# Performance work log

Measured on AMD Instinct MI355X. Metric: run time of the kernel, lower is better.

## Reference

```python
import jax, jax.numpy as jnp
import numpy as np

B, N, D = 16, 512, 256
HEADS = 8
HIDEF = 1024
BLOCK, WINDOW = 32, 64
LEVELS = 5
PYOUT = 128
NCLS, NANCH = 5, 9
NEG = -1e9


def _sinusoidal_pos(n, d):
    # PositionEmbeddingStatic: deterministic sinusoidal table [n, d]
    pos = np.arange(n)[:, None].astype(np.float64)
    i = np.arange(d)[None, :]
    angle = pos / np.power(10000.0, (2 * (i // 2)) / d)
    pe = np.where(i % 2 == 0, np.sin(angle), np.cos(angle))
    return jnp.asarray(pe, jnp.float32)


def _layernorm(x, g, b, eps=1e-5):
    m = x.mean(-1, keepdims=True)
    v = x.var(-1, keepdims=True)
    return (x - m) * jax.lax.rsqrt(v + eps) * g + b


def _bn(x_bcn, g, b, eps=1e-5):
    # BatchNorm1d in training mode: per-channel batch stats over (B, N)
    m = x_bcn.mean((0, 2), keepdims=True)
    v = x_bcn.var((0, 2), keepdims=True)
    return (x_bcn - m) * jax.lax.rsqrt(v + eps) * g[None, :, None] + b[None, :, None]


def _sparse_attention(x, Wqkv, bqkv, Wo, bo):
    # Windowed block-sparse attention: queries in block i attend to key blocks
    # [i-w, i+w] with w = window_size // block_size. Never materializes SxS.
    Bx, Nx, Dx = x.shape
    H, dh = HEADS, Dx // HEADS
    nb, bs = Nx // BLOCK, BLOCK
    w = WINDOW // BLOCK
    qkv = x @ Wqkv + bqkv
    q, k, v = jnp.split(qkv, 3, axis=-1)

    def to_blocks(t):  # [B,N,D] -> [B,H,nb,bs,dh]
        return t.reshape(Bx, nb, bs, H, dh).transpose(0, 3, 1, 2, 4)

    q, k, v = to_blocks(q), to_blocks(k), to_blocks(v)
    offs = list(range(-w, w + 1))
    # roll by -o puts key block (i+o) at query-block position i
    k_band = jnp.concatenate([jnp.roll(k, -o, axis=2) for o in offs], axis=3)
    v_band = jnp.concatenate([jnp.roll(v, -o, axis=2) for o in offs], axis=3)
    blk = jnp.arange(nb)
    valid = jnp.concatenate(
        [jnp.repeat(((blk + o >= 0) & (blk + o < nb))[:, None], bs, axis=1) for o in offs],
        axis=1)  # [nb, (2w+1)*bs]
    scale = 1.0 / jnp.sqrt(jnp.asarray(dh, x.dtype))
    scores = jnp.einsum('bhnqd,bhnkd->bhnqk', q, k_band) * scale
    scores = jnp.where(valid[None, None, :, None, :], scores, NEG)
    p = jax.nn.softmax(scores, axis=-1)
    o = jnp.einsum('bhnqk,bhnkd->bhnqd', p, v_band)
    o = o.transpose(0, 2, 3, 1, 4).reshape(Bx, Nx, Dx)
    return o @ Wo + bo


def setup_inputs():
    key = jax.random.key(0)
    ks = iter(jax.random.split(key, 48))
    g = lambda shape, s=0.02: jax.random.normal(next(ks), shape, jnp.float32) * s
    z = lambda *shape: jnp.zeros(shape, jnp.float32)
    o = lambda *shape: jnp.ones(shape, jnp.float32)
    return {
        'x': jax.random.normal(next(ks), (B, N, D), jnp.float32),
        'patch_W': g((D, D)), 'patch_b': z(D),
        'ln_g': o(D), 'ln_b': z(D),
        'ff_W1': g((D, HIDEF)), 'ff_b1': z(HIDEF),
        'ff_W2': g((HIDEF, D)), 'ff_b2': z(D),
        'Wqkv': g((D, 3 * D)), 'bqkv': z(3 * D),
        'Wo': g((D, D)), 'bo': z(D),
        'bn1_g': o(D), 'bn1_b': z(D),
        'bn2_g': o(D), 'bn2_b': z(D),
        'pyr_W': g((LEVELS, D, PYOUT)), 'pyr_b': z(LEVELS, PYOUT),
        'fcl_W': g((LEVELS * PYOUT * N, 128), 0.005), 'fcl_b': z(128),
        'addbn_g': o(128), 'addbn_b': z(128),
        'cls_W1': g((128, 256)), 'cls_b1': z(256),
        'cls_W2': g((256, NCLS * NANCH)), 'cls_b2': z(NCLS * NANCH),
        'box_W1': g((128, 128)), 'box_b1': z(128),
        'box_W2': g((128, 4 * NANCH)), 'box_b2': z(4 * NANCH),
    }


def reference(x, patch_W, patch_b, ln_g, ln_b, ff_W1, ff_b1, ff_W2, ff_b2,
              Wqkv, bqkv, Wo, bo, bn1_g, bn1_b, bn2_g, bn2_b,
              pyr_W, pyr_b, fcl_W, fcl_b, addbn_g, addbn_b,
              cls_W1, cls_b1, cls_W2, cls_b2, box_W1, box_b1, box_W2, box_b2):
    pos = _sinusoidal_pos(N, D)

    def ff(h):
        return jax.nn.gelu(h @ ff_W1 + ff_b1) @ ff_W2 + ff_b2

    def mnt(h):
        h = _layernorm(h @ patch_W + patch_b, ln_g, ln_b)  # patch embed + norm
        h = h + pos[None]
        idt = h
        h = ff(h)
        h = _sparse_attention(h, Wqkv, bqkv, Wo, bo)
        h = h + idt
        h = _bn(h.transpose(0, 2, 1), bn1_g, bn1_b).transpose(0, 2, 1)
        idt = h
        h = ff(h) + idt
        h = _bn(h.transpose(0, 2, 1), bn2_g, bn2_b).transpose(0, 2, 1)
        return h

    outs = []
    for _ in range(5):
        x = mnt(x)
        outs.append(x.transpose(0, 2, 1))  # [B, D, N]

    # pyramid: per-level 1x1 conv D -> 128
    feats = [jnp.einsum('bdn,dc->bcn', outs[i], pyr_W[i]) + pyr_b[i][None, :, None]
             for i in range(LEVELS)]
    flat = jnp.concatenate([f.reshape(f.shape[0], -1) for f in feats], axis=1)
    add = (flat @ fcl_W + fcl_b)[:, :, None]          # [B,128,1]
    add = _bn(add, addbn_g, addbn_b).transpose(0, 2, 1)  # [B,1,128]
    cls = jax.nn.relu(add @ cls_W1 + cls_b1) @ cls_W2 + cls_b2
    cls = jax.nn.softmax(cls, axis=-1).reshape(-1, NANCH, NCLS)  # eval mode softmax
    box = (jax.nn.relu(add @ box_W1 + box_b1) @ box_W2 + box_b2).reshape(-1, NANCH, 4)
    return jnp.concatenate([cls, box], axis=-1)  # [B, NANCH, NCLS+4]
```

## Files before the change

kernel.cpp:

```cpp
#include <hip/hip_runtime.h>
#include <hip/hip_bf16.h>
#include <math.h>

#define B_ 16
#define N_ 512
#define D_ 256
#define HEADS_ 8
#define DH_ 32
#define HIDEF_ 1024
#define NBLK_ 16
#define BS_ 32
#define LEVELS_ 5
#define PYOUT_ 128
#define ROWS_ (B_ * N_)
#define FCL_K 327680
#define FCL_KB 256
#define FCL_CHUNKS 1280

typedef __attribute__((ext_vector_type(8))) short short8;
typedef __attribute__((ext_vector_type(4))) short short4v;
typedef __attribute__((ext_vector_type(4))) unsigned short ushort4v;
typedef __attribute__((ext_vector_type(4))) float f32x4;

__device__ __forceinline__ float bf2f(short u) {
    return __uint_as_float(((unsigned int)(unsigned short)u) << 16);
}
__device__ __forceinline__ unsigned short f2bf(float x) {
    __hip_bfloat16 h = __float2bfloat16(x);
    return *reinterpret_cast<unsigned short*>(&h);
}

__global__ void pos_kernel(float* __restrict__ pos) {
    int idx = blockIdx.x * 256 + threadIdx.x;
    if (idx >= N_ * D_) return;
    int n = idx >> 8, i = idx & 255;
    double angle = (double)n / pow(10000.0, (double)(2 * (i >> 1)) / 256.0);
    pos[idx] = (float)((i & 1) ? cos(angle) : sin(angle));
}

__device__ __forceinline__ float gelu_f(float x) {
    float x3 = x * x * x;
    return 0.5f * x * (1.f + tanhf(0.7978845608028654f * (x + 0.044715f * x3)));
}

__global__ void tobf16_kernel(const float* __restrict__ x, __hip_bfloat16* __restrict__ y, int n) {
    int i = blockIdx.x * 256 + threadIdx.x;
    if (i < n) y[i] = __float2bfloat16(x[i]);
}

__global__ __launch_bounds__(256) void wconv_kernel(const float* __restrict__ W,
                                                    __hip_bfloat16* __restrict__ Wt,
                                                    int K, int N) {
    int z = blockIdx.z;
    const float* Wz = W + (size_t)z * K * N;
    __hip_bfloat16* Wtz = Wt + (size_t)z * K * N;
    __shared__ float t[32][33];
    int bx = blockIdx.x * 32, by = blockIdx.y * 32;
    int tx = threadIdx.x, ty = threadIdx.y;
#pragma unroll
    for (int i = 0; i < 32; i += 8)
        t[ty + i][tx] = Wz[(size_t)(by + ty + i) * N + bx + tx];
    __syncthreads();
#pragma unroll
    for (int i = 0; i < 32; i += 8)
        Wtz[(size_t)(bx + ty + i) * K + by + tx] = __float2bfloat16(t[tx][ty + i]);
}

template <int ACT, bool OUTF, bool OUTB, bool SCAT, bool STATS, int BN>
__global__ __launch_bounds__(256) void bgemm_kernel(
    const __hip_bfloat16* __restrict__ A, const __hip_bfloat16* __restrict__ Wt,
    const float* __restrict__ bias, const float* __restrict__ resid,
    float* __restrict__ C, __hip_bfloat16* __restrict__ Cb, int M, int Nn, int K,
    int level, float* __restrict__ bnp) {
    __shared__ __hip_bfloat16 Alds[128 * 32];
    __shared__ __hip_bfloat16 Blds[BN * 32];
    constexpr int MW = (BN == 128) ? 4 : 2;
    constexpr int WH = (BN == 128) ? 64 : 32;
    constexpr int BR = BN / 64;
    int tid = threadIdx.x;
    int wid = tid >> 6, lane = tid & 63;
    int row0 = blockIdx.y * 128, col0 = blockIdx.x * BN;
    int wr = (BN == 128) ? (wid >> 1) : wid;
    int wc = (BN == 128) ? (wid & 1) : 0;
    int r16 = lane & 15, kq = lane >> 4;
    int rdoff = kq ^ ((r16 >> 1) & 3);

    f32x4 acc[MW][4];
#pragma unroll
    for (int m = 0; m < MW; m++)
#pragma unroll
        for (int n = 0; n < 4; n++) acc[m][n] = (f32x4){0.f, 0.f, 0.f, 0.f};

    for (int k0 = 0; k0 < K; k0 += 32) {
#pragma unroll
        for (int i = 0; i < 2; i++) {
            int slot = i * 256 + tid;
            int row = slot >> 2, qp = slot & 3;
            int q = qp ^ ((row >> 1) & 3);
            const __hip_bfloat16* ga = A + (size_t)(row0 + row) * K + k0 + q * 8;
            __builtin_amdgcn_global_load_lds(
                (const __attribute__((address_space(1))) void*)ga,
                (__attribute__((address_space(3))) void*)((char*)Alds + i * 4096 + wid * 1024),
                16, 0, 0);
        }
#pragma unroll
        for (int i = 0; i < BR; i++) {
            int slot = i * 256 + tid;
            int row = slot >> 2, qp = slot & 3;
            int q = qp ^ ((row >> 1) & 3);
            const __hip_bfloat16* gb = Wt + (size_t)(col0 + row) * K + k0 + q * 8;
            __builtin_amdgcn_global_load_lds(
                (const __attribute__((address_space(1))) void*)gb,
                (__attribute__((address_space(3))) void*)((char*)Blds + i * 4096 + wid * 1024),
                16, 0, 0);
        }
        __syncthreads();
        short8 af[MW], bf[4];
#pragma unroll
        for (int m = 0; m < MW; m++) {
            int row = wr * WH + m * 16 + r16;
            af[m] = *reinterpret_cast<const short8*>(
                reinterpret_cast<const char*>(Alds) + row * 64 + rdoff * 16);
        }
#pragma unroll
        for (int n = 0; n < 4; n++) {
            int row = wc * 64 + n * 16 + r16;
            bf[n] = *reinterpret_cast<const short8*>(
                reinterpret_cast<const char*>(Blds) + row * 64 + rdoff * 16);
        }
#pragma unroll
        for (int m = 0; m < MW; m++)
#pragma unroll
            for (int n = 0; n < 4; n++)
                acc[m][n] = __builtin_amdgcn_mfma_f32_16x16x32_bf16(af[m], bf[n], acc[m][n], 0, 0, 0);
        __syncthreads();
    }

    int rg = lane >> 4;
    float s1a[4] = {0.f, 0.f, 0.f, 0.f}, s2a[4] = {0.f, 0.f, 0.f, 0.f};
    if (SCAT) {
#pragma unroll
        for (int n = 0; n < 4; n++) {
            int cc = col0 + wc * 64 + n * 16 + r16;
            int bb = cc >> 9, nn = cc & 511;
            float* dst = C + (size_t)bb * (LEVELS_ * PYOUT_ * N_) +
                         (size_t)level * PYOUT_ * N_ + nn;
#pragma unroll
            for (int m = 0; m < MW; m++) {
                int rbase = wr * WH + m * 16 + rg * 4;
#pragma unroll
                for (int j = 0; j < 4; j++) {
                    int ch = rbase + j;
                    dst[(size_t)ch * N_] = acc[m][n][j] + bias[ch];
                }
            }
        }
    } else {
#pragma unroll
        for (int n = 0; n < 4; n++) {
            int cc = col0 + wc * 64 + n * 16 + r16;
            float bv = bias[cc];
#pragma unroll
            for (int m = 0; m < MW; m++) {
                int rb = row0 + wr * WH + m * 16 + rg * 4;
#pragma unroll
                for (int j = 0; j < 4; j++) {
                    int r = rb + j;
                    float v = acc[m][n][j] + bv;
                    if (resid) v += resid[(size_t)r * Nn + cc];
                    if (ACT == 1) v = gelu_f(v);
                    if (OUTF) C[(size_t)r * Nn + cc] = v;
                    if (OUTB) Cb[(size_t)r * Nn + cc] = __float2bfloat16(v);
                    if (STATS) { s1a[n] += v; s2a[n] += v * v; }
                }
            }
        }
    }
    if (STATS) {
        float* sc = (float*)Alds;
        int part = wid * 4 + rg;
#pragma unroll
        for (int n = 0; n < 4; n++) {
            int c = wc * 64 + n * 16 + r16;
            sc[c * 16 + part] = s1a[n];
            sc[1024 + c * 16 + part] = s2a[n];
        }
        __syncthreads();
        if (tid < BN) {
            float a = 0.f, b2 = 0.f;
#pragma unroll
            for (int p = 0; p < 16; p++) {
                a += sc[tid * 16 + p];
                b2 += sc[1024 + tid * 16 + p];
            }
            bnp[blockIdx.y * 256 + col0 + tid] = a;
            bnp[16384 + blockIdx.y * 256 + col0 + tid] = b2;
        }
    }
}

__global__ __launch_bounds__(256) void patchln_kernel(
    const __hip_bfloat16* __restrict__ A, const __hip_bfloat16* __restrict__ Wt,
    const float* __restrict__ bias, const float* __restrict__ lng,
    const float* __restrict__ lnb, const float* __restrict__ pos,
    float* __restrict__ H, __hip_bfloat16* __restrict__ Hb) {
    __shared__ char __attribute__((aligned(16))) smem[33280];
    __hip_bfloat16* Alds = (__hip_bfloat16*)smem;
    __hip_bfloat16* Blds = (__hip_bfloat16*)(smem + 2048);
    float (*Cls)[260] = (float(*)[260])smem;
    int tid = threadIdx.x;
    int wid = tid >> 6, lane = tid & 63;
    int row0 = blockIdx.x * 32;
    int r16 = lane & 15, kq = lane >> 4, g = lane >> 4;
    int rdoff = kq ^ ((r16 >> 1) & 3);

    f32x4 acc[2][4];
#pragma unroll
    for (int m = 0; m < 2; m++)
#pragma unroll
        for (int n = 0; n < 4; n++) acc[m][n] = (f32x4){0.f, 0.f, 0.f, 0.f};

    for (int k0 = 0; k0 < 256; k0 += 32) {
        if (tid < 128) {
            int row = tid >> 2, qp = tid & 3;
            int q = qp ^ ((row >> 1) & 3);
            const __hip_bfloat16* ga = A + (size_t)(row0 + row) * 256 + k0 + q * 8;
            __builtin_amdgcn_global_load_lds(
                (const __attribute__((address_space(1))) void*)ga,
                (__attribute__((address_space(3))) void*)((char*)Alds + wid * 1024),
                16, 0, 0);
        }
#pragma unroll
        for (int i = 0; i < 4; i++) {
            int slot = i * 256 + tid;
            int row = slot >> 2, qp = slot & 3;
            int q = qp ^ ((row >> 1) & 3);
            const __hip_bfloat16* gb = Wt + (size_t)row * 256 + k0 + q * 8;
            __builtin_amdgcn_global_load_lds(
                (const __attribute__((address_space(1))) void*)gb,
                (__attribute__((address_space(3))) void*)((char*)Blds + i * 4096 + wid * 1024),
                16, 0, 0);
        }
        __syncthreads();
        short8 af[2], bf[4];
#pragma unroll
        for (int m = 0; m < 2; m++) {
            int row = m * 16 + r16;
            af[m] = *reinterpret_cast<const short8*>(
                reinterpret_cast<const char*>(Alds) + row * 64 + rdoff * 16);
        }
#pragma unroll
        for (int n = 0; n < 4; n++) {
            int row = wid * 64 + n * 16 + r16;
            bf[n] = *reinterpret_cast<const short8*>(
                reinterpret_cast<const char*>(Blds) + row * 64 + rdoff * 16);
        }
#pragma unroll
        for (int m = 0; m < 2; m++)
#pragma unroll
            for (int n = 0; n < 4; n++)
                acc[m][n] = __builtin_amdgcn_mfma_f32_16x16x32_bf16(af[m], bf[n], acc[m][n], 0, 0, 0);
        __syncthreads();
    }
#pragma unroll
    for (int n = 0; n < 4; n++) {
        int col = wid * 64 + n * 16 + r16;
        float bv = bias[col];
#pragma unroll
        for (int m = 0; m < 2; m++)
#pragma unroll
            for (int j = 0; j < 4; j++)
                Cls[m * 16 + g * 4 + j][col] = acc[m][n][j] + bv;
    }
    __syncthreads();
    float4 g4 = ((const float4*)lng)[lane];
    float4 b4 = ((const float4*)lnb)[lane];
#pragma unroll
    for (int rr = 0; rr < 8; rr++) {
        int r = wid * 8 + rr;
        float4 v = *(const float4*)&Cls[r][lane * 4];
        float s = v.x + v.y + v.z + v.w;
#pragma unroll
        for (int mk = 32; mk; mk >>= 1) s += __shfl_xor(s, mk);
        float mean = s * (1.f / 256.f);
        float dx = v.x - mean, dy = v.y - mean, dz = v.z - mean, dw = v.w - mean;
        float q = dx * dx + dy * dy + dz * dz + dw * dw;
#pragma unroll
        for (int mk = 32; mk; mk >>= 1) q += __shfl_xor(q, mk);
        float rstd = rsqrtf(q * (1.f / 256.f) + 1e-5f);
        int grow = row0 + r;
        float4 p4 = ((const float4*)pos)[(size_t)(grow & (N_ - 1)) * 64 + lane];
        float o0 = dx * rstd * g4.x + b4.x + p4.x;
        float o1 = dy * rstd * g4.y + b4.y + p4.y;
        float o2 = dz * rstd * g4.z + b4.z + p4.z;
        float o3 = dw * rstd * g4.w + b4.w + p4.w;
        ((float4*)(H + (size_t)grow * D_))[lane] = (float4){o0, o1, o2, o3};
        ushort4v u = {f2bf(o0), f2bf(o1), f2bf(o2), f2bf(o3)};
        *((ushort4v*)(Hb + (size_t)grow * D_) + lane) = u;
    }
}

__global__ __launch_bounds__(256) void bn_applyfin_kernel(
    const float* __restrict__ x, const float* __restrict__ bnp,
    const float* __restrict__ g, const float* __restrict__ b,
    float* __restrict__ y, __hip_bfloat16* __restrict__ yb) {
    int tid = threadIdx.x;
    __shared__ float sm[256], sv[256];
    {
        float s = 0.f, s2 = 0.f;
#pragma unroll 4
        for (int yy = 0; yy < 64; yy++) {
            s += bnp[yy * 256 + tid];
            s2 += bnp[16384 + yy * 256 + tid];
        }
        float m = s * (1.f / 8192.f);
        sm[tid] = m;
        sv[tid] = rsqrtf(s2 * (1.f / 8192.f) - m * m + 1e-5f);
    }
    __syncthreads();
    int lane = tid & 63, w = tid >> 6;
    int row0 = blockIdx.x * 32;
    float4 m4 = *(const float4*)&sm[lane * 4];
    float4 r4 = *(const float4*)&sv[lane * 4];
    float4 g4 = ((const float4*)g)[lane];
    float4 b4 = ((const float4*)b)[lane];
#pragma unroll
    for (int rr = 0; rr < 8; rr++) {
        int row = row0 + w * 8 + rr;
        float4 x4 = ((const float4*)(x + (size_t)row * D_))[lane];
        float o0 = (x4.x - m4.x) * r4.x * g4.x + b4.x;
        float o1 = (x4.y - m4.y) * r4.y * g4.y + b4.y;
        float o2 = (x4.z - m4.z) * r4.z * g4.z + b4.z;
        float o3 = (x4.w - m4.w) * r4.w * g4.w + b4.w;
        if (y) ((float4*)(y + (size_t)row * D_))[lane] = (float4){o0, o1, o2, o3};
        if (yb) {
            ushort4v u = {f2bf(o0), f2bf(o1), f2bf(o2), f2bf(o3)};
            *((ushort4v*)(yb + (size_t)row * D_) + lane) = u;
        }
    }
}

__global__ __launch_bounds__(256) void attn_kernel(
    const __hip_bfloat16* __restrict__ qkv, __hip_bfloat16* __restrict__ outb) {
    int bx = blockIdx.x, h = blockIdx.y, b = blockIdx.z;
    int tid = threadIdx.x;
    int wid = tid >> 6, lane = tid & 63;
    __shared__ __hip_bfloat16 Klds[256 * 32];
    __shared__ __hip_bfloat16 Vt[32 * 264];
    const short* q16 = (const short*)qkv;

#pragma unroll
    for (int r = 0; r < 4; r++) {
        int slot = r * 256 + tid;
        int row = slot >> 2, qp = slot & 3;
        int ql = qp ^ ((row >> 1) & 3);
        int jb = bx * 4 - 2 + (row >> 5);
        jb = jb < 0 ? 0 : (jb > 15 ? 15 : jb);
        const short* ga = q16 + ((size_t)(b * N_ + jb * 32 + (row & 31))) * 768 + 256 + h * 32 + ql * 8;
        __builtin_amdgcn_global_load_lds(
            (const __attribute__((address_space(1))) void*)ga,
            (__attribute__((address_space(3))) void*)((char*)Klds + r * 4096 + wid * 1024),
            16, 0, 0);
    }
    {
        int row = tid;
        int jb = bx * 4 - 2 + (row >> 5);
        jb = jb < 0 ? 0 : (jb > 15 ? 15 : jb);
        const short* gv = q16 + ((size_t)(b * N_ + jb * 32 + (row & 31))) * 768 + 512 + h * 32;
        short8 v0 = *(const short8*)(gv);
        short8 v1 = *(const short8*)(gv + 8);
        short8 v2 = *(const short8*)(gv + 16);
        short8 v3 = *(const short8*)(gv + 24);
        short* vt = (short*)Vt;
#pragma unroll
        for (int e = 0; e < 8; e++) {
            vt[(e) * 264 + row] = v0[e];
            vt[(8 + e) * 264 + row] = v1[e];
            vt[(16 + e) * 264 + row] = v2[e];
            vt[(24 + e) * 264 + row] = v3[e];
        }
    }
    __syncthreads();

    int i = bx * 4 + wid;
    int c = lane & 15, g = lane >> 4;
    const float scale = 0.17677669529663687f;

#pragma unroll
    for (int qt = 0; qt < 2; qt++) {
        const short* qa = q16 + ((size_t)(b * N_ + i * 32 + qt * 16 + c)) * 768 + h * 32 + g * 8;
        short8 bq = *(const short8*)qa;
        f32x4 st[10];
#pragma unroll
        for (int t = 0; t < 10; t++) {
            int jb = i - 2 + (t >> 1);
            if (jb >= 0 && jb < NBLK_) {
                int row = wid * 32 + t * 16 + c;
                int phys = g ^ ((row >> 1) & 3);
                short8 ak = *(const short8*)((const char*)Klds + row * 64 + phys * 16);
                st[t] = __builtin_amdgcn_mfma_f32_16x16x32_bf16(
                    ak, bq, (f32x4){0.f, 0.f, 0.f, 0.f}, 0, 0, 0);
            }
        }
        float mx = -1e30f;
#pragma unroll
        for (int t = 0; t < 10; t++) {
            int jb = i - 2 + (t >> 1);
            if (jb >= 0 && jb < NBLK_) {
#pragma unroll
                for (int j = 0; j < 4; j++) {
                    st[t][j] *= scale;
                    mx = fmaxf(mx, st[t][j]);
                }
            }
        }
        mx = fmaxf(mx, __shfl_xor(mx, 16));
        mx = fmaxf(mx, __shfl_xor(mx, 32));
        float sum = 0.f;
#pragma unroll
        for (int t = 0; t < 10; t++) {
            int jb = i - 2 + (t >> 1);
            if (jb >= 0 && jb < NBLK_) {
#pragma unroll
                for (int j = 0; j < 4; j++) {
                    float e = __expf(st[t][j] - mx);
                    st[t][j] = e;
                    sum += e;
                }
            }
        }
        sum += __shfl_xor(sum, 16);
        sum += __shfl_xor(sum, 32);
        float inv = 1.f / sum;
        f32x4 o0 = (f32x4){0.f, 0.f, 0.f, 0.f};
        f32x4 o1 = (f32x4){0.f, 0.f, 0.f, 0.f};
        const short* vt = (const short*)Vt;
#pragma unroll
        for (int t = 0; t < 10; t++) {
            int jb = i - 2 + (t >> 1);
            if (jb >= 0 && jb < NBLK_) {
                short8 pa = (short8)0;
#pragma unroll
                for (int j = 0; j < 4; j++) pa[j] = (short)f2bf(st[t][j] * inv);
                int kb = wid * 32 + t * 16 + g * 4;
                short4v vb0 = *(const short4v*)(vt + (0 * 16 + c) * 264 + kb);
                short4v vb1 = *(const short4v*)(vt + (1 * 16 + c) * 264 + kb);
                short8 b0 = (short8)0, b1 = (short8)0;
#pragma unroll
                for (int e = 0; e < 4; e++) { b0[e] = vb0[e]; b1[e] = vb1[e]; }
                o0 = __builtin_amdgcn_mfma_f32_16x16x32_bf16(pa, b0, o0, 0, 0, 0);
                o1 = __builtin_amdgcn_mfma_f32_16x16x32_bf16(pa, b1, o1, 0, 0, 0);
            }
        }
#pragma unroll
        for (int j = 0; j < 4; j++) {
            size_t rbase = ((size_t)(b * N_ + i * 32 + qt * 16 + g * 4 + j)) * D_ + h * DH_;
            outb[rbase + c] = __float2bfloat16(o0[j]);
            outb[rbase + 16 + c] = __float2bfloat16(o1[j]);
        }
    }
}

__global__ __launch_bounds__(256) void fcl_partial_kernel(
    const float* __restrict__ flat, const float* __restrict__ W,
    float* __restrict__ partial) {
    int chunk = blockIdx.x;
    int t = threadIdx.x;
    int k0 = chunk * FCL_KB;
    __shared__ float fl[FCL_KB][20];
#pragma unroll
    for (int b = 0; b < 16; b++)
        fl[t][b] = flat[(size_t)b * FCL_K + k0 + t];
    __syncthreads();
    int j = t & 127, bg = t >> 7;
    f32x4 a0 = (f32x4){0.f, 0.f, 0.f, 0.f};
    f32x4 a1 = (f32x4){0.f, 0.f, 0.f, 0.f};
#pragma unroll 8
    for (int k = 0; k < FCL_KB; k++) {
        float w = W[(size_t)(k0 + k) * 128 + j];
        f32x4 f0 = *(const f32x4*)&fl[k][bg * 8];
        f32x4 f1 = *(const f32x4*)&fl[k][bg * 8 + 4];
        a0 += f0 * w;
        a1 += f1 * w;
    }
#pragma unroll
    for (int bi = 0; bi < 4; bi++) {
        partial[((size_t)chunk * 16 + bg * 8 + bi) * 128 + j] = a0[bi];
        partial[((size_t)chunk * 16 + bg * 8 + 4 + bi) * 128 + j] = a1[bi];
    }
}

__global__ __launch_bounds__(256) void fcl_reduce_kernel(
    const float* __restrict__ partial, const float* __restrict__ fcl_b,
    float* __restrict__ add) {
    int c0 = blockIdx.x * 32;
    int t = threadIdx.x;
    int ry = t >> 5, cx = t & 31;
    float s = 0.f;
    for (int r = ry; r < FCL_CHUNKS; r += 8)
        s += partial[(size_t)r * 2048 + c0 + cx];
    __shared__ float red[8][32];
    red[ry][cx] = s; __syncthreads();
    if (ry == 0) {
        float tot = 0.f;
#pragma unroll
        for (int q = 0; q < 8; q++) tot += red[q][cx];
        int col = c0 + cx;
        add[col] = tot + fcl_b[col & 127];
    }
}

__global__ __launch_bounds__(256) void head_kernel(
    const float* __restrict__ add, const float* __restrict__ abg, const float* __restrict__ abb,
    const float* __restrict__ cls_W1, const float* __restrict__ cls_b1,
    const float* __restrict__ cls_W2, const float* __restrict__ cls_b2,
    const float* __restrict__ box_W1, const float* __restrict__ box_b1,
    const float* __restrict__ box_W2, const float* __restrict__ box_b2,
    float* __restrict__ out) {
    __shared__ float a2[16][128];
    __shared__ float cm[16][256];
    __shared__ float cls[16][45];
    __shared__ float bmid[16][128];
    __shared__ float smden[16];
    int t = threadIdx.x;
    if (t < 128) {
        float m = 0.f;
#pragma unroll
        for (int b = 0; b < 16; b++) m += add[b * 128 + t];
        m *= (1.f / 16.f);
        float v = 0.f;
#pragma unroll
        for (int b = 0; b < 16; b++) { float d = add[b * 128 + t] - m; v += d * d; }
        v *= (1.f / 16.f);
        float sc = rsqrtf(v + 1e-5f) * abg[t];
#pragma unroll
        for (int b = 0; b < 16; b++) a2[b][t] = (add[b * 128 + t] - m) * sc + abb[t];
    }
    __syncthreads();
    for (int idx = t; idx < 4096; idx += 256) {
        int m = idx >> 8, c = idx & 255;
        float a = cls_b1[c];
        for (int k = 0; k < 128; k++) a += a2[m][k] * cls_W1[k * 256 + c];
        cm[m][c] = fmaxf(a, 0.f);
    }
    for (int idx = t; idx < 2048; idx += 256) {
        int m = idx >> 7, c = idx & 127;
        float a = box_b1[c];
        for (int k = 0; k < 128; k++) a += a2[m][k] * box_W1[k * 128 + c];
        bmid[m][c] = fmaxf(a, 0.f);
    }
    __syncthreads();
    for (int idx = t; idx < 720; idx += 256) {
        int m = idx / 45, c = idx % 45;
        float a = cls_b2[c];
        for (int k = 0; k < 256; k++) a += cm[m][k] * cls_W2[k * 45 + c];
        cls[m][c] = a;
    }
    __syncthreads();
    if (t < 16) {
        float mx = -1e30f;
        for (int c = 0; c < 45; c++) mx = fmaxf(mx, cls[t][c]);
        float s = 0.f;
        for (int c = 0; c < 45; c++) { float e = expf(cls[t][c] - mx); cls[t][c] = e; s += e; }
        smden[t] = s;
    }
    for (int idx = t; idx < 576; idx += 256) {
        int m = idx / 36, c = idx % 36;
        float a = box_b2[c];
        for (int k = 0; k < 128; k++) a += bmid[m][k] * box_W2[k * 36 + c];
        out[m * 81 + (c >> 2) * 9 + 5 + (c & 3)] = a;
    }
    __syncthreads();
    for (int idx = t; idx < 720; idx += 256) {
        int m = idx / 45, c = idx % 45;
        out[m * 81 + (c / 5) * 9 + (c % 5)] = cls[m][c] / smden[m];
    }
}

extern "C" void kernel_launch(void* const* d_in, const int* in_sizes, int n_in,
                              void* d_out, int out_size, void* d_ws, size_t ws_size,
                              hipStream_t stream) {
    const float* x_in    = (const float*)d_in[0];
    const float* patch_W = (const float*)d_in[1];
    const float* patch_b = (const float*)d_in[2];
    const float* ln_g    = (const float*)d_in[3];
    const float* ln_b    = (const float*)d_in[4];
    const float* ff_W1   = (const float*)d_in[5];
    const float* ff_b1   = (const float*)d_in[6];
    const float* ff_W2   = (const float*)d_in[7];
    const float* ff_b2   = (const float*)d_in[8];
    const float* Wqkv    = (const float*)d_in[9];
    const float* bqkv    = (const float*)d_in[10];
    const float* Wo      = (const float*)d_in[11];
    const float* bo      = (const float*)d_in[12];
    const float* bn1_g   = (const float*)d_in[13];
    const float* bn1_b   = (const float*)d_in[14];
    const float* bn2_g   = (const float*)d_in[15];
    const float* bn2_b   = (const float*)d_in[16];
    const float* pyr_W   = (const float*)d_in[17];
    const float* pyr_b   = (const float*)d_in[18];
    const float* fcl_W   = (const float*)d_in[19];
    const float* fcl_b   = (const float*)d_in[20];
    const float* addbn_g = (const float*)d_in[21];
    const float* addbn_b = (const float*)d_in[22];
    const float* cls_W1  = (const float*)d_in[23];
    const float* cls_b1  = (const float*)d_in[24];
    const float* cls_W2  = (const float*)d_in[25];
    const float* cls_b2  = (const float*)d_in[26];
    const float* box_W1  = (const float*)d_in[27];
    const float* box_b1  = (const float*)d_in[28];
    const float* box_W2  = (const float*)d_in[29];
    const float* box_b2  = (const float*)d_in[30];
    float* out = (float*)d_out;

    float* ws = (float*)d_ws;
    size_t off = 0;
    float* POS   = ws + off; off += 131072;
    float* H     = ws + off; off += 2097152;
    float* T     = ws + off; off += 2097152;
    float* UNION = ws + off; off += 4194304;
    float* FLAT  = ws + off; off += 5242880;
    float* PART  = ws + off; off += (size_t)FCL_CHUNKS * 2048;
    float* STATS = ws + off; off += 512;
    float* BNP   = ws + off; off += 2 * 64 * 256;
    float* ADD   = ws + off; off += 2048;
    __hip_bfloat16* Hb   = (__hip_bfloat16*)(ws + off); off += 1048576;
    __hip_bfloat16* Tb   = (__hip_bfloat16*)(ws + off); off += 1048576;
    __hip_bfloat16* Xb   = (__hip_bfloat16*)(ws + off); off += 1048576;
    __hip_bfloat16* ATb  = (__hip_bfloat16*)(ws + off); off += 1048576;
    __hip_bfloat16* patchWt = (__hip_bfloat16*)(ws + off); off += 32768;
    __hip_bfloat16* qkvWt   = (__hip_bfloat16*)(ws + off); off += 98304;
    __hip_bfloat16* WoWt    = (__hip_bfloat16*)(ws + off); off += 32768;
    __hip_bfloat16* W1t     = (__hip_bfloat16*)(ws + off); off += 131072;
    __hip_bfloat16* W2t     = (__hip_bfloat16*)(ws + off); off += 131072;
    __hip_bfloat16* pyrWt   = (__hip_bfloat16*)(ws + off); off += 81920;
    __hip_bfloat16* MIDb = (__hip_bfloat16*)UNION;
    __hip_bfloat16* QKVb = (__hip_bfloat16*)UNION;
    (void)STATS;

    pos_kernel<<<(N_ * D_ + 255) / 256, 256, 0, stream>>>(POS);
    wconv_kernel<<<dim3(D_ / 32, D_ / 32, 1), dim3(32, 8), 0, stream>>>(patch_W, patchWt, D_, D_);
    wconv_kernel<<<dim3(768 / 32, D_ / 32, 1), dim3(32, 8), 0, stream>>>(Wqkv, qkvWt, D_, 768);
    wconv_kernel<<<dim3(D_ / 32, D_ / 32, 1), dim3(32, 8), 0, stream>>>(Wo, WoWt, D_, D_);
    wconv_kernel<<<dim3(HIDEF_ / 32, D_ / 32, 1), dim3(32, 8), 0, stream>>>(ff_W1, W1t, D_, HIDEF_);
    wconv_kernel<<<dim3(D_ / 32, HIDEF_ / 32, 1), dim3(32, 8), 0, stream>>>(ff_W2, W2t, HIDEF_, D_);
    wconv_kernel<<<dim3(PYOUT_ / 32, D_ / 32, LEVELS_), dim3(32, 8), 0, stream>>>(pyr_W, pyrWt, D_, PYOUT_);
    tobf16_kernel<<<(ROWS_ * D_ + 255) / 256, 256, 0, stream>>>(x_in, Xb, ROWS_ * D_);

    for (int it = 0; it < 5; it++) {
        patchln_kernel<<<256, 256, 0, stream>>>(Xb, patchWt, patch_b, ln_g, ln_b, POS, H, Hb);
        bgemm_kernel<1, false, true, false, false, 128><<<dim3(8, 64), 256, 0, stream>>>(
            Hb, W1t, ff_b1, nullptr, nullptr, MIDb, ROWS_, HIDEF_, D_, 0, nullptr);
        bgemm_kernel<0, false, true, false, false, 64><<<dim3(4, 64), 256, 0, stream>>>(
            MIDb, W2t, ff_b2, nullptr, nullptr, Tb, ROWS_, D_, HIDEF_, 0, nullptr);
        bgemm_kernel<0, false, true, false, false, 128><<<dim3(6, 64), 256, 0, stream>>>(
            Tb, qkvWt, bqkv, nullptr, nullptr, QKVb, ROWS_, 768, D_, 0, nullptr);
        attn_kernel<<<dim3(4, HEADS_, B_), 256, 0, stream>>>(QKVb, ATb);
        bgemm_kernel<0, true, false, false, true, 64><<<dim3(4, 64), 256, 0, stream>>>(
            ATb, WoWt, bo, H, T, nullptr, ROWS_, D_, D_, 0, BNP);
        bn_applyfin_kernel<<<256, 256, 0, stream>>>(T, BNP, bn1_g, bn1_b, H, Hb);
        bgemm_kernel<1, false, true, false, false, 128><<<dim3(8, 64), 256, 0, stream>>>(
            Hb, W1t, ff_b1, nullptr, nullptr, MIDb, ROWS_, HIDEF_, D_, 0, nullptr);
        bgemm_kernel<0, true, false, false, true, 64><<<dim3(4, 64), 256, 0, stream>>>(
            MIDb, W2t, ff_b2, H, T, nullptr, ROWS_, D_, HIDEF_, 0, BNP);
        bn_applyfin_kernel<<<256, 256, 0, stream>>>(T, BNP, bn2_g, bn2_b, nullptr, Xb);
        bgemm_kernel<0, false, false, true, false, 64><<<dim3(128, 1), 256, 0, stream>>>(
            pyrWt + (size_t)it * D_ * PYOUT_, Xb, pyr_b + it * PYOUT_, nullptr,
            FLAT, nullptr, PYOUT_, ROWS_, D_, it, nullptr);
    }

    fcl_partial_kernel<<<FCL_CHUNKS, 256, 0, stream>>>(FLAT, fcl_W, PART);
    fcl_reduce_kernel<<<64, 256, 0, stream>>>(PART, fcl_b, ADD);
    head_kernel<<<1, 256, 0, stream>>>(ADD, addbn_g, addbn_b,
        cls_W1, cls_b1, cls_W2, cls_b2, box_W1, box_b1, box_W2, box_b2, out);
    (void)in_sizes; (void)n_in; (void)out_size; (void)ws_size;
}
```

Baseline: 1.004 ms.

## Double GEMM K-tile to 64 and merge prep kernels into one launch

The bf16 GEMM and patch-LN kernels now stage 64-wide K tiles in LDS, with an 8-way XOR swizzle and two MFMA sub-steps per tile. This halves the number of barrier pairs and loop iterations per K pass, at the cost of more LDS per block, which can reduce occupancy. The eight setup launches (positional table, six weight transposes, input cast) are folded into a single prep kernel that dispatches by block index. The input cast is also vectorized.

```diff
diff --git a/kernel.cpp b/kernel.cpp
--- a/kernel.cpp
+++ b/kernel.cpp
@@ -30,40 +30,58 @@
     return *reinterpret_cast<unsigned short*>(&h);
 }
 
-__global__ void pos_kernel(float* __restrict__ pos) {
-    int idx = blockIdx.x * 256 + threadIdx.x;
-    if (idx >= N_ * D_) return;
-    int n = idx >> 8, i = idx & 255;
-    double angle = (double)n / pow(10000.0, (double)(2 * (i >> 1)) / 256.0);
-    pos[idx] = (float)((i & 1) ? cos(angle) : sin(angle));
-}
-
 __device__ __forceinline__ float gelu_f(float x) {
     float x3 = x * x * x;
     return 0.5f * x * (1.f + tanhf(0.7978845608028654f * (x + 0.044715f * x3)));
 }
 
-__global__ void tobf16_kernel(const float* __restrict__ x, __hip_bfloat16* __restrict__ y, int n) {
-    int i = blockIdx.x * 256 + threadIdx.x;
-    if (i < n) y[i] = __float2bfloat16(x[i]);
-}
-
-__global__ __launch_bounds__(256) void wconv_kernel(const float* __restrict__ W,
-                                                    __hip_bfloat16* __restrict__ Wt,
-                                                    int K, int N) {
-    int z = blockIdx.z;
-    const float* Wz = W + (size_t)z * K * N;
-    __hip_bfloat16* Wtz = Wt + (size_t)z * K * N;
-    __shared__ float t[32][33];
-    int bx = blockIdx.x * 32, by = blockIdx.y * 32;
-    int tx = threadIdx.x, ty = threadIdx.y;
+__global__ __launch_bounds__(256) void prep_kernel(
+    const float* __restrict__ patch_W, const float* __restrict__ Wqkv,
+    const float* __restrict__ Wo, const float* __restrict__ ff_W1,
+    const float* __restrict__ ff_W2, const float* __restrict__ pyr_W,
+    const float* __restrict__ x_in,
+    __hip_bfloat16* __restrict__ patchWt, __hip_bfloat16* __restrict__ qkvWt,
+    __hip_bfloat16* __restrict__ WoWt, __hip_bfloat16* __restrict__ W1t,
+    __hip_bfloat16* __restrict__ W2t, __hip_bfloat16* __restrict__ pyrWt,
+    float* __restrict__ pos, __hip_bfloat16* __restrict__ Xb) {
+    __shared__ float tt[32][33];
+    int bid = blockIdx.x, t = threadIdx.x;
+    if (bid >= 1504) {
+        int base = (bid - 1504) * 2048 + t * 8;
+        float4 a = *(const float4*)&x_in[base];
+        float4 b = *(const float4*)&x_in[base + 4];
+        ushort4v u0 = {f2bf(a.x), f2bf(a.y), f2bf(a.z), f2bf(a.w)};
+        ushort4v u1 = {f2bf(b.x), f2bf(b.y), f2bf(b.z), f2bf(b.w)};
+        *(ushort4v*)((short*)Xb + base) = u0;
+        *(ushort4v*)((short*)Xb + base + 4) = u1;
+        return;
+    }
+    if (bid >= 992) {
+        int idx = (bid - 992) * 256 + t;
+        int n = idx >> 8, i = idx & 255;
+        double angle = (double)n / pow(10000.0, (double)(2 * (i >> 1)) / 256.0);
+        pos[idx] = (float)((i & 1) ? cos(angle) : sin(angle));
+        return;
+    }
+    const float* W; __hip_bfloat16* Wt; int K, N, bx, by;
+    if (bid < 64)       { W = patch_W; Wt = patchWt; K = 256; N = 256; bx = bid % 8; by = bid / 8; }
+    else if (bid < 256) { int l = bid - 64;  W = Wqkv;  Wt = qkvWt; K = 256; N = 768;  bx = l % 24; by = l / 24; }
+    else if (bid < 320) { int l = bid - 256; W = Wo;    Wt = WoWt;  K = 256; N = 256;  bx = l % 8;  by = l / 8; }
+    else if (bid < 576) { int l = bid - 320; W = ff_W1; Wt = W1t;   K = 256; N = 1024; bx = l % 32; by = l / 32; }
+    else if (bid < 832) { int l = bid - 576; W = ff_W2; Wt = W2t;   K = 1024; N = 256; bx = l % 8;  by = l / 32 * 4 + (l / 8) % 4; }
+    else                { int l = bid - 832; int z = l / 32; int r = l % 32;
+                          W = pyr_W + (size_t)z * 256 * 128; Wt = pyrWt + (size_t)z * 256 * 128;
+                          K = 256; N = 128; bx = r % 4; by = r / 4; }
+    if (bid >= 576 && bid < 832) { int l = bid - 576; bx = l % 8; by = l / 8; }
+    int bx32 = bx * 32, by32 = by * 32;
+    int tx = t & 31, ty = t >> 5;
 #pragma unroll
     for (int i = 0; i < 32; i += 8)
-        t[ty + i][tx] = Wz[(size_t)(by + ty + i) * N + bx + tx];
+        tt[ty + i][tx] = W[(size_t)(by32 + ty + i) * N + bx32 + tx];
     __syncthreads();
 #pragma unroll
     for (int i = 0; i < 32; i += 8)
-        Wtz[(size_t)(bx + ty + i) * K + by + tx] = __float2bfloat16(t[tx][ty + i]);
+        Wt[(size_t)(bx32 + ty + i) * K + by32 + tx] = __float2bfloat16(tt[tx][ty + i]);
 }
 
 template <int ACT, bool OUTF, bool OUTB, bool SCAT, bool STATS, int BN>
@@ -72,18 +90,17 @@
     const float* __restrict__ bias, const float* __restrict__ resid,
     float* __restrict__ C, __hip_bfloat16* __restrict__ Cb, int M, int Nn, int K,
     int level, float* __restrict__ bnp) {
-    __shared__ __hip_bfloat16 Alds[128 * 32];
-    __shared__ __hip_bfloat16 Blds[BN * 32];
+    __shared__ __hip_bfloat16 Alds[128 * 64];
+    __shared__ __hip_bfloat16 Blds[BN * 64];
     constexpr int MW = (BN == 128) ? 4 : 2;
     constexpr int WH = (BN == 128) ? 64 : 32;
-    constexpr int BR = BN / 64;
+    constexpr int BR = BN / 32;
     int tid = threadIdx.x;
     int wid = tid >> 6, lane = tid & 63;
     int row0 = blockIdx.y * 128, col0 = blockIdx.x * BN;
     int wr = (BN == 128) ? (wid >> 1) : wid;
     int wc = (BN == 128) ? (wid & 1) : 0;
     int r16 = lane & 15, kq = lane >> 4;
-    int rdoff = kq ^ ((r16 >> 1) & 3);
 
     f32x4 acc[MW][4];
 #pragma unroll
@@ -91,12 +108,12 @@
 #pragma unroll
         for (int n = 0; n < 4; n++) acc[m][n] = (f32x4){0.f, 0.f, 0.f, 0.f};
 
-    for (int k0 = 0; k0 < K; k0 += 32) {
-#pragma unroll
-        for (int i = 0; i < 2; i++) {
+    for (int k0 = 0; k0 < K; k0 += 64) {
+#pragma unroll
+        for (int i = 0; i < 4; i++) {
             int slot = i * 256 + tid;
-            int row = slot >> 2, qp = slot & 3;
-            int q = qp ^ ((row >> 1) & 3);
+            int row = slot >> 3, qp = slot & 7;
+            int q = qp ^ ((row >> 1) & 7);
             const __hip_bfloat16* ga = A + (size_t)(row0 + row) * K + k0 + q * 8;
             __builtin_amdgcn_global_load_lds(
                 (const __attribute__((address_space(1))) void*)ga,
@@ -106,8 +123,8 @@
 #pragma unroll
         for (int i = 0; i < BR; i++) {
             int slot = i * 256 + tid;
-            int row = slot >> 2, qp = slot & 3;
-            int q = qp ^ ((row >> 1) & 3);
+            int row = slot >> 3, qp = slot & 7;
+            int q = qp ^ ((row >> 1) & 7);
             const __hip_bfloat16* gb = Wt + (size_t)(col0 + row) * K + k0 + q * 8;
             __builtin_amdgcn_global_load_lds(
                 (const __attribute__((address_space(1))) void*)gb,
@@ -115,24 +132,29 @@
                 16, 0, 0);
         }
         __syncthreads();
-        short8 af[MW], bf[4];
-#pragma unroll
-        for (int m = 0; m < MW; m++) {
-            int row = wr * WH + m * 16 + r16;
-            af[m] = *reinterpret_cast<const short8*>(
-                reinterpret_cast<const char*>(Alds) + row * 64 + rdoff * 16);
-        }
-#pragma unroll
-        for (int n = 0; n < 4; n++) {
-            int row = wc * 64 + n * 16 + r16;
-            bf[n] = *reinterpret_cast<const short8*>(
-                reinterpret_cast<const char*>(Blds) + row * 64 + rdoff * 16);
-        }
-#pragma unroll
-        for (int m = 0; m < MW; m++)
-#pragma unroll
-            for (int n = 0; n < 4; n++)
-                acc[m][n] = __builtin_amdgcn_mfma_f32_16x16x32_bf16(af[m], bf[n], acc[m][n], 0, 0, 0);
+#pragma unroll
+        for (int h = 0; h < 2; h++) {
+            short8 af[MW], bf4[4];
+#pragma unroll
+            for (int m = 0; m < MW; m++) {
+                int row = wr * WH + m * 16 + r16;
+                int phys = (h * 4 + kq) ^ ((row >> 1) & 7);
+                af[m] = *reinterpret_cast<const short8*>(
+                    reinterpret_cast<const char*>(Alds) + row * 128 + phys * 16);
+            }
+#pragma unroll
+            for (int n = 0; n < 4; n++) {
+                int row = wc * 64 + n * 16 + r16;
+                int phys = (h * 4 + kq) ^ ((row >> 1) & 7);
+                bf4[n] = *reinterpret_cast<const short8*>(
+                    reinterpret_cast<const char*>(Blds) + row * 128 + phys * 16);
+            }
+#pragma unroll
+            for (int m = 0; m < MW; m++)
+#pragma unroll
+                for (int n = 0; n < 4; n++)
+                    acc[m][n] = __builtin_amdgcn_mfma_f32_16x16x32_bf16(af[m], bf4[n], acc[m][n], 0, 0, 0);
+        }
         __syncthreads();
     }
 
@@ -183,7 +205,7 @@
         for (int n = 0; n < 4; n++) {
             int c = wc * 64 + n * 16 + r16;
             sc[c * 16 + part] = s1a[n];
-            sc[1024 + c * 16 + part] = s2a[n];
+            sc[BN * 16 + c * 16 + part] = s2a[n];
         }
         __syncthreads();
         if (tid < BN) {
@@ -191,7 +213,7 @@
 #pragma unroll
             for (int p = 0; p < 16; p++) {
                 a += sc[tid * 16 + p];
-                b2 += sc[1024 + tid * 16 + p];
+                b2 += sc[BN * 16 + tid * 16 + p];
             }
             bnp[blockIdx.y * 256 + col0 + tid] = a;
             bnp[16384 + blockIdx.y * 256 + col0 + tid] = b2;
@@ -204,15 +226,14 @@
     const float* __restrict__ bias, const float* __restrict__ lng,
     const float* __restrict__ lnb, const float* __restrict__ pos,
     float* __restrict__ H, __hip_bfloat16* __restrict__ Hb) {
-    __shared__ char __attribute__((aligned(16))) smem[33280];
+    __shared__ char __attribute__((aligned(16))) smem[36864];
     __hip_bfloat16* Alds = (__hip_bfloat16*)smem;
-    __hip_bfloat16* Blds = (__hip_bfloat16*)(smem + 2048);
+    __hip_bfloat16* Blds = (__hip_bfloat16*)(smem + 4096);
     float (*Cls)[260] = (float(*)[260])smem;
     int tid = threadIdx.x;
     int wid = tid >> 6, lane = tid & 63;
     int row0 = blockIdx.x * 32;
     int r16 = lane & 15, kq = lane >> 4, g = lane >> 4;
-    int rdoff = kq ^ ((r16 >> 1) & 3);
 
     f32x4 acc[2][4];
 #pragma unroll
@@ -220,10 +241,10 @@
 #pragma unroll
         for (int n = 0; n < 4; n++) acc[m][n] = (f32x4){0.f, 0.f, 0.f, 0.f};
 
-    for (int k0 = 0; k0 < 256; k0 += 32) {
-        if (tid < 128) {
-            int row = tid >> 2, qp = tid & 3;
-            int q = qp ^ ((row >> 1) & 3);
+    for (int k0 = 0; k0 < 256; k0 += 64) {
+        {
+            int row = tid >> 3, qp = tid & 7;
+            int q = qp ^ ((row >> 1) & 7);
             const __hip_bfloat16* ga = A + (size_t)(row0 + row) * 256 + k0 + q * 8;
             __builtin_amdgcn_global_load_lds(
                 (const __attribute__((address_space(1))) void*)ga,
@@ -231,10 +252,10 @@
                 16, 0, 0);
         }
 #pragma unroll
-        for (int i = 0; i < 4; i++) {
+        for (int i = 0; i < 8; i++) {
             int slot = i * 256 + tid;
-            int row = slot >> 2, qp = slot & 3;
-            int q = qp ^ ((row >> 1) & 3);
+            int row = slot >> 3, qp = slot & 7;
+            int q = qp ^ ((row >> 1) & 7);
             const __hip_bfloat16* gb = Wt + (size_t)row * 256 + k0 + q * 8;
             __builtin_amdgcn_global_load_lds(
                 (const __attribute__((address_space(1))) void*)gb,
@@ -242,24 +263,29 @@
                 16, 0, 0);
         }
         __syncthreads();
-        short8 af[2], bf[4];
-#pragma unroll
-        for (int m = 0; m < 2; m++) {
-            int row = m * 16 + r16;
-            af[m] = *reinterpret_cast<const short8*>(
-                reinterpret_cast<const char*>(Alds) + row * 64 + rdoff * 16);
-        }
-#pragma unroll
-        for (int n = 0; n < 4; n++) {
-            int row = wid * 64 + n * 16 + r16;
-            bf[n] = *reinterpret_cast<const short8*>(
-                reinterpret_cast<const char*>(Blds) + row * 64 + rdoff * 16);
-        }
-#pragma unroll
-        for (int m = 0; m < 2; m++)
-#pragma unroll
-            for (int n = 0; n < 4; n++)
-                acc[m][n] = __builtin_amdgcn_mfma_f32_16x16x32_bf16(af[m], bf[n], acc[m][n], 0, 0, 0);
+#pragma unroll
+        for (int h = 0; h < 2; h++) {
+            short8 af[2], bf4[4];
+#pragma unroll
+            for (int m = 0; m < 2; m++) {
+                int row = m * 16 + r16;
+                int phys = (h * 4 + kq) ^ ((row >> 1) & 7);
+                af[m] = *reinterpret_cast<const short8*>(
+                    reinterpret_cast<const char*>(Alds) + row * 128 + phys * 16);
+            }
+#pragma unroll
+            for (int n = 0; n < 4; n++) {
+                int row = wid * 64 + n * 16 + r16;
+                int phys = (h * 4 + kq) ^ ((row >> 1) & 7);
+                bf4[n] = *reinterpret_cast<const short8*>(
+                    reinterpret_cast<const char*>(Blds) + row * 128 + phys * 16);
+            }
+#pragma unroll
+            for (int m = 0; m < 2; m++)
+#pragma unroll
+                for (int n = 0; n < 4; n++)
+                    acc[m][n] = __builtin_amdgcn_mfma_f32_16x16x32_bf16(af[m], bf4[n], acc[m][n], 0, 0, 0);
+        }
         __syncthreads();
     }
 #pragma unroll
@@ -621,7 +647,6 @@
     float* UNION = ws + off; off += 4194304;
     float* FLAT  = ws + off; off += 5242880;
     float* PART  = ws + off; off += (size_t)FCL_CHUNKS * 2048;
-    float* STATS = ws + off; off += 512;
     float* BNP   = ws + off; off += 2 * 64 * 256;
     float* ADD   = ws + off; off += 2048;
     __hip_bfloat16* Hb   = (__hip_bfloat16*)(ws + off); off += 1048576;
@@ -636,16 +661,10 @@
     __hip_bfloat16* pyrWt   = (__hip_bfloat16*)(ws + off); off += 81920;
     __hip_bfloat16* MIDb = (__hip_bfloat16*)UNION;
     __hip_bfloat16* QKVb = (__hip_bfloat16*)UNION;
-    (void)STATS;
-
-    pos_kernel<<<(N_ * D_ + 255) / 256, 256, 0, stream>>>(POS);
-    wconv_kernel<<<dim3(D_ / 32, D_ / 32, 1), dim3(32, 8), 0, stream>>>(patch_W, patchWt, D_, D_);
-    wconv_kernel<<<dim3(768 / 32, D_ / 32, 1), dim3(32, 8), 0, stream>>>(Wqkv, qkvWt, D_, 768);
-    wconv_kernel<<<dim3(D_ / 32, D_ / 32, 1), dim3(32, 8), 0, stream>>>(Wo, WoWt, D_, D_);
-    wconv_kernel<<<dim3(HIDEF_ / 32, D_ / 32, 1), dim3(32, 8), 0, stream>>>(ff_W1, W1t, D_, HIDEF_);
-    wconv_kernel<<<dim3(D_ / 32, HIDEF_ / 32, 1), dim3(32, 8), 0, stream>>>(ff_W2, W2t, HIDEF_, D_);
-    wconv_kernel<<<dim3(PYOUT_ / 32, D_ / 32, LEVELS_), dim3(32, 8), 0, stream>>>(pyr_W, pyrWt, D_, PYOUT_);
-    tobf16_kernel<<<(ROWS_ * D_ + 255) / 256, 256, 0, stream>>>(x_in, Xb, ROWS_ * D_);
+
+    prep_kernel<<<2528, 256, 0, stream>>>(
+        patch_W, Wqkv, Wo, ff_W1, ff_W2, pyr_W, x_in,
+        patchWt, qkvWt, WoWt, W1t, W2t, pyrWt, POS, Xb);
 
     for (int it = 0; it < 5; it++) {
         patchln_kernel<<<256, 256, 0, stream>>>(Xb, patchWt, patch_b, ln_g, ln_b, POS, H, Hb);
```

New measurement: 972.2 us. 3.1% less time.
